# Optimization experiments

Measured on AMD Instinct MI355X. Metric: run time of the kernel, lower is better.

## Reference

```python
import jax, jax.numpy as jnp
import numpy as np

FG_THR = 0.7
BG_THR = 0.3
NUM_PER_IMAGE = 256
NUM_POS_MAX = int(NUM_PER_IMAGE * 0.5)  # positive_ratio = 0.5
BBOX_W = (1.0, 1.0, 1.0, 1.0)
BETA = 1.0 / 9.0


def _permute(t, C):
    # N x (A*C) x H x W -> N x (H*W*A) x C, matching RPNLoss.permute
    N, _, H, W = t.shape
    t = t.reshape(N, -1, C, H, W)
    t = jnp.transpose(t, (0, 3, 4, 1, 2))
    return t.reshape(N, -1, C)


def _iou(a, b):
    # a: [N,4], b: [M,4] -> [N,M] (with +1 box convention, as in source)
    x_tl = jnp.maximum(a[:, None, 0], b[None, :, 0])
    y_tl = jnp.maximum(a[:, None, 1], b[None, :, 1])
    x_rb = jnp.minimum(a[:, None, 2], b[None, :, 2])
    y_rb = jnp.minimum(a[:, None, 3], b[None, :, 3])
    inter = jnp.clip(x_rb - x_tl + 1.0, 0.0) * jnp.clip(y_rb - y_tl + 1.0, 0.0)
    area1 = (a[:, 2] - a[:, 0] + 1.0) * (a[:, 3] - a[:, 1] + 1.0)
    area2 = (b[:, 2] - b[:, 0] + 1.0) * (b[:, 3] - b[:, 1] + 1.0)
    return inter / (area1[:, None] + area2[None, :] - inter)


def _encode(anchors, targets):
    ws = anchors[:, 2] - anchors[:, 0] + 1.0
    hs = anchors[:, 3] - anchors[:, 1] + 1.0
    x_ctr = anchors[:, 0] + 0.5 * ws
    y_ctr = anchors[:, 1] + 0.5 * hs
    t_ws = targets[:, 2] - targets[:, 0] + 1.0
    t_hs = targets[:, 3] - targets[:, 1] + 1.0
    t_x = targets[:, 0] + 0.5 * t_ws
    t_y = targets[:, 1] + 0.5 * t_hs
    wx, wy, ww, wh = BBOX_W
    tx = wx * (t_x - x_ctr) / ws
    ty = wy * (t_y - y_ctr) / hs
    tw = ww * jnp.log(t_ws / ws)
    th = wh * jnp.log(t_hs / hs)
    return jnp.stack([tx, ty, tw, th], axis=1)


def _bce_logits(l, t):
    return jnp.maximum(l, 0.0) - l * t + jnp.log1p(jnp.exp(-jnp.abs(l)))


def _per_image(anchor, logit, breg, size, target, key):
    N = anchor.shape[0]
    ious = _iou(anchor, target)  # [N, M]
    vals = ious.max(axis=1)
    ori = jnp.argmax(ious, axis=1).astype(jnp.int32)
    inds = jnp.where(vals < BG_THR, -1, ori)
    inds = jnp.where((vals >= BG_THR) & (vals < FG_THR), -2, inds)
    # low-quality matches: anchors achieving the per-target max IoU keep their argmax
    col_max = ious.max(axis=0)
    restore = (ious == col_max[None, :]).any(axis=1)
    inds = jnp.where(restore, ori, inds)
    # filter_anchors: keep anchors fully inside the image (size = (h, w))
    inside = (anchor[:, 0] >= 0) & (anchor[:, 1] >= 0) & \
             (anchor[:, 2] <= size[1] - 1.0) & (anchor[:, 3] <= size[0] - 1.0)
    inds = jnp.where(inside, inds, -2)

    pos = inds >= 0
    neg = inds == -1
    # random sampling via random priorities + fixed-size top_k with validity masks
    r = jax.random.uniform(key, (N,))
    pos_vals, pos_idx = jax.lax.top_k(jnp.where(pos, r, -1.0), NUM_POS_MAX)
    valid_pos = pos_vals >= 0.0
    num_pos = valid_pos.sum()
    neg_vals, neg_idx = jax.lax.top_k(jnp.where(neg, r, -1.0), NUM_PER_IMAGE)
    valid_neg = (neg_vals >= 0.0) & (jnp.arange(NUM_PER_IMAGE) < (NUM_PER_IMAGE - num_pos))

    # classification loss terms (BCE with logits); pos target 1, neg target 0
    vp = valid_pos.astype(logit.dtype)
    vn = valid_neg.astype(logit.dtype)
    cls_sum = jnp.sum(_bce_logits(logit[pos_idx], 1.0) * vp) + \
              jnp.sum(_bce_logits(logit[neg_idx], 0.0) * vn)
    count = num_pos + valid_neg.sum()

    m = jnp.clip(inds[pos_idx], 0, None)
    offsets = _encode(anchor[pos_idx], target[m])
    diff = jnp.abs(breg[pos_idx] - offsets)
    sl1 = jnp.where(diff < BETA, 0.5 * diff * diff / BETA, diff - 0.5 * BETA)
    reg_sum = jnp.sum(sl1 * vp[:, None])
    return cls_sum, count, reg_sum


def reference(anchors, logits, bbox_regs, sizes, targets):
    B = anchors.shape[0]
    log = _permute(logits, 1)[..., 0]      # [B, H*W*A]
    breg = _permute(bbox_regs, 4)          # [B, H*W*A, 4]
    keys = jax.random.split(jax.random.key(42), B)
    cls_s, cnt, reg_s = jax.vmap(_per_image)(anchors, log, breg, sizes, targets, keys)
    total = jnp.sum(cnt).astype(anchors.dtype)
    cls_loss = jnp.sum(cls_s) / total
    reg_loss = jnp.sum(reg_s) / total
    return jnp.stack([cls_loss, reg_loss])


def setup_inputs() -> dict:
    key = jax.random.key(0)
    ks = jax.random.split(key, 10)
    B, A, H, W, M = 4, 3, 168, 256, 32
    N = H * W * A
    IMG_H, IMG_W = 800.0, 1333.0
    x1 = jax.random.uniform(ks[0], (B, N)) * 1200.0
    y1 = jax.random.uniform(ks[1], (B, N)) * 700.0
    aw = jax.random.uniform(ks[2], (B, N)) * 300.0 + 16.0
    ah = jax.random.uniform(ks[3], (B, N)) * 300.0 + 16.0
    anchors = jnp.stack([x1, y1, x1 + aw, y1 + ah], axis=-1)  # some out of image -> filtered
    tx1 = jax.random.uniform(ks[4], (B, M)) * 1000.0
    ty1 = jax.random.uniform(ks[5], (B, M)) * 500.0
    tw = jax.random.uniform(ks[6], (B, M)) * 250.0 + 30.0
    th = jax.random.uniform(ks[7], (B, M)) * 200.0 + 30.0
    targets = jnp.stack([tx1, ty1, jnp.minimum(tx1 + tw, IMG_W - 1.0),
                         jnp.minimum(ty1 + th, IMG_H - 1.0)], axis=-1)
    logits = jax.random.normal(ks[8], (B, A, H, W), dtype=jnp.float32)
    bbox_regs = jax.random.normal(ks[9], (B, 4 * A, H, W), dtype=jnp.float32) * 0.1
    sizes = jnp.tile(jnp.array([IMG_H, IMG_W], dtype=jnp.float32), (B, 1))
    return {"anchors": anchors, "logits": logits, "bbox_regs": bbox_regs,
            "sizes": sizes, "targets": targets}
```

## Files before the change

### kernel.cpp

```cpp
#include <hip/hip_runtime.h>
#include <stdint.h>

#define Bn 4
#define An 3
#define Hn 168
#define Wn 256
#define Mn 32
#define HWn (Hn*Wn)
#define Nn (HWn*An)
#define POS_CAP 8192
#define BND_CAP 2048
#define NPERIM 256
#define NPOSMAX 128
#define FG_THR 0.7f
#define BG_THR 0.3f
#define BETA (1.0f/9.0f)

#define NBLK 126
#define APT 4
#define STRIDE (NBLK * 256)
#define SEG 1024
#define WPI (NBLK * 4)
#define HB 256
#define HSH 15
#define BSEGCAP 64

#define OFF_POSCNT 0
#define OFF_BOUND  8
#define OFF_NEED   12
#define OFF_COUNT  16
#define OFF_CLS    17
#define OFF_REG    18
#define OFF_KEYS   24
#define OFF_WMAX   32
#define OFF_PACKED 64544
#define OFF_NSEGC  1096736
#define OFF_BSEGC  1097240
#define OFF_PHIST  1097744
#define OFF_PLIST  1226768
#define OFF_BSEG   1292304
#define OFF_NLIST  1356816

__device__ __forceinline__ uint32_t rotl32(uint32_t v, int n) { return (v << n) | (v >> (32 - n)); }

__device__ __forceinline__ void tf2x32(uint32_t k0, uint32_t k1, uint32_t x0, uint32_t x1,
                                       uint32_t& o0, uint32_t& o1) {
    uint32_t k2 = k0 ^ k1 ^ 0x1BD11BDAu;
    x0 += k0; x1 += k1;
    x0 += x1; x1 = rotl32(x1, 13); x1 ^= x0;
    x0 += x1; x1 = rotl32(x1, 15); x1 ^= x0;
    x0 += x1; x1 = rotl32(x1, 26); x1 ^= x0;
    x0 += x1; x1 = rotl32(x1, 6);  x1 ^= x0;
    x0 += k1; x1 += k2 + 1u;
    x0 += x1; x1 = rotl32(x1, 17); x1 ^= x0;
    x0 += x1; x1 = rotl32(x1, 29); x1 ^= x0;
    x0 += x1; x1 = rotl32(x1, 16); x1 ^= x0;
    x0 += x1; x1 = rotl32(x1, 24); x1 ^= x0;
    x0 += k2; x1 += k0 + 2u;
    x0 += x1; x1 = rotl32(x1, 13); x1 ^= x0;
    x0 += x1; x1 = rotl32(x1, 15); x1 ^= x0;
    x0 += x1; x1 = rotl32(x1, 26); x1 ^= x0;
    x0 += x1; x1 = rotl32(x1, 6);  x1 ^= x0;
    x0 += k0; x1 += k1 + 3u;
    x0 += x1; x1 = rotl32(x1, 17); x1 ^= x0;
    x0 += x1; x1 = rotl32(x1, 29); x1 ^= x0;
    x0 += x1; x1 = rotl32(x1, 16); x1 ^= x0;
    x0 += x1; x1 = rotl32(x1, 24); x1 ^= x0;
    x0 += k1; x1 += k2 + 4u;
    x0 += x1; x1 = rotl32(x1, 13); x1 ^= x0;
    x0 += x1; x1 = rotl32(x1, 15); x1 ^= x0;
    x0 += x1; x1 = rotl32(x1, 26); x1 ^= x0;
    x0 += x1; x1 = rotl32(x1, 6);  x1 ^= x0;
    x0 += k2; x1 += k0 + 5u;
    o0 = x0; o1 = x1;
}

__device__ __forceinline__ uint32_t rng_m23(uint32_t k0, uint32_t k1, uint32_t i) {
    uint32_t o0, o1;
    tf2x32(k0, k1, 0u, i, o0, o1);
    return (o0 ^ o1) >> 9;
}

__device__ __forceinline__ float iou_one(float a0, float a1, float a2, float a3,
                                         float t0, float t1, float t2, float t3) {
    float xtl = fmaxf(a0, t0), ytl = fmaxf(a1, t1);
    float xrb = fminf(a2, t2), yrb = fminf(a3, t3);
    float iw = fmaxf(xrb - xtl + 1.0f, 0.0f);
    float ih = fmaxf(yrb - ytl + 1.0f, 0.0f);
    float inter = iw * ih;
    float area1 = (a2 - a0 + 1.0f) * (a3 - a1 + 1.0f);
    float area2 = (t2 - t0 + 1.0f) * (t3 - t1 + 1.0f);
    return inter * __builtin_amdgcn_rcpf(area1 + area2 - inter);
}

__global__ void __launch_bounds__(256) k1_colmax(const float* __restrict__ anchors,
                                                 const float* __restrict__ targets,
                                                 const float* __restrict__ sizes,
                                                 uint32_t* __restrict__ ws) {
    int b = blockIdx.y, j = blockIdx.x, tid = threadIdx.x;
    if (b == 0 && j == 0) {
        if (tid < 24) ws[tid] = 0u;
        if (tid == 0) {
            for (int bb = 0; bb < Bn; ++bb) {
                uint32_t o0, o1;
                tf2x32(0u, 42u, 0u, (uint32_t)bb, o0, o1);
                ws[OFF_KEYS + 2*bb] = o0; ws[OFF_KEYS + 2*bb + 1] = o1;
            }
        }
    }
    int lane = tid & 63;
    int w = j * 4 + (tid >> 6);
    int base = j * 256 + tid;
    float4 a[APT];
    #pragma unroll
    for (int k = 0; k < APT; ++k)
        a[k] = ((const float4*)anchors)[b * Nn + base + k * STRIDE];
    float rowmax[APT]; int ori[APT]; uint32_t eqm[APT];
    #pragma unroll
    for (int k = 0; k < APT; ++k) { rowmax[k] = -1.0f; ori[k] = 0; eqm[k] = 0u; }
    float mywm = 0.0f;
    #pragma unroll 4
    for (int t = 0; t < Mn; ++t) {
        float4 tv = ((const float4*)targets)[b * Mn + t];
        float iou[APT];
        float m0 = 0.0f;
        #pragma unroll
        for (int k = 0; k < APT; ++k) {
            iou[k] = iou_one(a[k].x, a[k].y, a[k].z, a[k].w, tv.x, tv.y, tv.z, tv.w);
            if (iou[k] > rowmax[k]) { rowmax[k] = iou[k]; ori[k] = t; }
            m0 = fmaxf(m0, iou[k]);
        }
        #pragma unroll
        for (int o = 32; o > 0; o >>= 1) m0 = fmaxf(m0, __shfl_xor(m0, o, 64));
        #pragma unroll
        for (int k = 0; k < APT; ++k)
            eqm[k] |= (iou[k] == m0) ? (1u << t) : 0u;
        mywm = (lane == t) ? m0 : mywm;
    }
    if (lane < Mn)
        ws[OFF_WMAX + ((size_t)b * WPI + w) * Mn + lane] = __float_as_uint(mywm);
    float sh = sizes[b * 2 + 0], sw = sizes[b * 2 + 1];
    #pragma unroll
    for (int k = 0; k < APT; ++k) {
        int i = base + k * STRIDE;
        uint32_t inside = (a[k].x >= 0.0f) && (a[k].y >= 0.0f) &&
                          (a[k].z <= sw - 1.0f) && (a[k].w <= sh - 1.0f);
        uint32_t flags = (uint32_t)ori[k] | (inside << 5) |
                         ((rowmax[k] >= FG_THR ? 1u : 0u) << 6) |
                         ((rowmax[k] <  BG_THR ? 1u : 0u) << 7);
        ((uint2*)(ws + OFF_PACKED))[(size_t)b * Nn + i] = make_uint2(eqm[k], flags);
    }
}

__global__ void __launch_bounds__(256) k2_cat(uint32_t* __restrict__ ws) {
    int b = blockIdx.y, j = blockIdx.x, tid = threadIdx.x;
    int lane = tid & 63;
    int w = j * 4 + (tid >> 6);
    __shared__ float cmf[Mn];
    __shared__ float redf[256];
    __shared__ uint32_t lh[HB];
    __shared__ uint32_t segcnt;
    {
        int t = tid & 31, sub = tid >> 5;
        float acc = 0.0f;
        for (int ww = sub; ww < WPI; ww += 8)
            acc = fmaxf(acc, __uint_as_float(ws[OFF_WMAX + ((size_t)b * WPI + ww) * Mn + t]));
        redf[tid] = acc;
        __syncthreads();
        if (sub == 0) {
            #pragma unroll
            for (int q = 1; q < 8; ++q) acc = fmaxf(acc, redf[t + 32 * q]);
            cmf[t] = acc;
        }
    }
    lh[tid] = 0u;
    if (tid == 0) segcnt = 0u;
    __syncthreads();
    float wmv = (lane < Mn)
        ? __uint_as_float(ws[OFF_WMAX + ((size_t)b * WPI + w) * Mn + lane]) : -1.0f;
    float cmv = (lane < Mn) ? cmf[lane] : 0.0f;
    uint32_t gmask = (uint32_t)__ballot(lane < Mn && wmv == cmv);

    uint32_t key0 = ws[OFF_KEYS + 2 * b], key1 = ws[OFF_KEYS + 2 * b + 1];
    unsigned long long lt_mask = (lane == 63) ? 0x7FFFFFFFFFFFFFFFull : ((1ull << lane) - 1ull);
    uint2* nseg = (uint2*)(ws + OFF_NLIST) + (size_t)(b * NBLK + j) * SEG;
    int base = j * 256 + tid;
    #pragma unroll
    for (int k = 0; k < APT; ++k) {
        int i = base + k * STRIDE;
        uint2 pk = ((const uint2*)(ws + OFF_PACKED))[(size_t)b * Nn + i];
        uint32_t ori = pk.y & 31u;
        bool inside = (pk.y >> 5) & 1u;
        bool gefg   = (pk.y >> 6) & 1u;
        bool ltbg   = (pk.y >> 7) & 1u;
        bool restore = (pk.x & gmask) != 0u;
        uint32_t cat = 0;
        if (inside) {
            if (restore || gefg) cat = 2;
            else if (ltbg) cat = 1;
        }
        uint32_t m = rng_m23(key0, key1, (uint32_t)i);
        unsigned long long pmask = __ballot(cat == 2u);
        if (pmask) {
            int leader = __ffsll((long long)pmask) - 1;
            uint32_t bb = 0;
            if (lane == leader) bb = atomicAdd(&ws[OFF_POSCNT + b], (uint32_t)__popcll(pmask));
            bb = __shfl(bb, leader, 64);
            if (cat == 2u) {
                uint32_t p = bb + (uint32_t)__popcll(pmask & lt_mask);
                if (p < POS_CAP)
                    ((uint2*)(ws + OFF_PLIST))[(size_t)b * POS_CAP + p] =
                        make_uint2(m, (uint32_t)i | (ori << 17));
            }
        }
        unsigned long long nmask = __ballot(cat == 1u);
        if (nmask) {
            int leader = __ffsll((long long)nmask) - 1;
            uint32_t bb = 0;
            if (lane == leader) bb = atomicAdd(&segcnt, (uint32_t)__popcll(nmask));
            bb = __shfl(bb, leader, 64);
            if (cat == 1u) {
                uint32_t p = bb + (uint32_t)__popcll(nmask & lt_mask);
                nseg[p] = make_uint2(m, (uint32_t)i);
                atomicAdd(&lh[m >> HSH], 1u);
            }
        }
    }
    __syncthreads();
    ws[OFF_PHIST + ((size_t)b * NBLK + j) * HB + tid] = lh[tid];
    if (tid == 0) ws[OFF_NSEGC + b * NBLK + j] = segcnt;
}

__global__ void __launch_bounds__(256) k25_bound(uint32_t* __restrict__ ws) {
    int b = blockIdx.x, t = threadIdx.x;
    __shared__ uint32_t csum[256];
    const uint32_t* ph = ws + OFF_PHIST + (size_t)b * NBLK * HB;
    uint32_t h = 0;
    for (int s = 0; s < NBLK; ++s) h += ph[s * HB + t];
    csum[t] = h;
    __syncthreads();
    for (int off = 1; off < 256; off <<= 1) {
        uint32_t mine = csum[t];
        uint32_t add = (t + off < 256) ? csum[t + off] : 0u;
        __syncthreads();
        csum[t] = mine + add;
        __syncthreads();
    }
    uint32_t pc = ws[OFF_POSCNT + b];
    int num_pos = (pc < (uint32_t)NPOSMAX) ? (int)pc : NPOSMAX;
    int k_neg = NPERIM - num_pos;
    uint32_t total = csum[0];
    if ((int)total < k_neg) {
        if (t == 0) {
            ws[OFF_BOUND + b] = 0xFFFFFFFFu;
            ws[OFF_NEED + b] = 0u;
            atomicAdd(&ws[OFF_COUNT], (uint32_t)(num_pos + (int)total));
        }
        return;
    }
    uint32_t incl = csum[t];
    uint32_t next = (t < 255) ? csum[t + 1] : 0u;
    if ((int)incl >= k_neg && (int)next < k_neg) {
        ws[OFF_BOUND + b] = (uint32_t)t;
        ws[OFF_NEED + b] = (uint32_t)(k_neg - (int)next);
        atomicAdd(&ws[OFF_COUNT], (uint32_t)(num_pos + k_neg));
    }
}

__global__ void __launch_bounds__(256) k3_neg(const float* __restrict__ logits,
                                              uint32_t* __restrict__ ws) {
    int b = blockIdx.y, j = blockIdx.x;
    int tid = threadIdx.x;
    __shared__ uint32_t bcnt;
    __shared__ float red[256];
    if (tid == 0) bcnt = 0u;
    __syncthreads();
    int bd = (int)(int32_t)ws[OFF_BOUND + b];
    int cnt = (int)ws[OFF_NSEGC + b * NBLK + j];
    const uint2* nseg = (const uint2*)(ws + OFF_NLIST) + (size_t)(b * NBLK + j) * SEG;
    uint2* bseg = (uint2*)(ws + OFF_BSEG) + (size_t)(b * NBLK + j) * BSEGCAP;
    float local = 0.0f;
    for (int idx = tid; idx < cnt; idx += 256) {
        uint2 e = nseg[idx];
        int bk = (int)(e.x >> HSH);
        if (bk > bd) {
            int i = (int)e.y;
            int a = i % An, hw = i / An;
            float l = logits[(b * An + a) * HWn + hw];
            local += fmaxf(l, 0.0f) + log1pf(expf(-fabsf(l)));
        } else if (bk == bd) {
            uint32_t q = atomicAdd(&bcnt, 1u);
            if (q < BSEGCAP) bseg[q] = e;
        }
    }
    red[tid] = local;
    __syncthreads();
    for (int s = 128; s > 0; s >>= 1) {
        if (tid < s) red[tid] += red[tid + s];
        __syncthreads();
    }
    if (tid == 0) {
        if (red[0] != 0.0f) atomicAdd((float*)&ws[OFF_CLS], red[0]);
        ws[OFF_BSEGC + b * NBLK + j] = (bcnt < BSEGCAP) ? bcnt : BSEGCAP;
    }
}

__device__ __forceinline__ bool sel_less(uint2 a, uint2 b) {
    return (a.x > b.x) || (a.x == b.x && a.y < b.y);
}

__device__ void bitonic_sort_shared(uint2* buf, int n) {
    for (int k = 2; k <= n; k <<= 1) {
        for (int j = k >> 1; j > 0; j >>= 1) {
            for (int t = (int)threadIdx.x; t < n; t += 256) {
                int ixj = t ^ j;
                if (ixj > t) {
                    uint2 x = buf[t], y = buf[ixj];
                    bool up = ((t & k) == 0);
                    bool sw = up ? sel_less(y, x) : sel_less(x, y);
                    if (sw) { buf[t] = y; buf[ixj] = x; }
                }
            }
            __syncthreads();
        }
    }
}

__global__ void __launch_bounds__(256) k4_final(const float* __restrict__ anchors,
                                                const float* __restrict__ targets,
                                                const float* __restrict__ logits,
                                                const float* __restrict__ bregs,
                                                uint32_t* __restrict__ ws) {
    int b = blockIdx.x, tid = threadIdx.x;
    __shared__ uint2 buf[BND_CAP];
    __shared__ float red[256];
    __shared__ uint32_t pre[128];
    float cls = 0.0f, reg = 0.0f;

    uint32_t pcu = ws[OFF_POSCNT + b];
    int pc = (pcu < (uint32_t)POS_CAP) ? (int)pcu : POS_CAP;
    const uint2* plist = (const uint2*)(ws + OFF_PLIST) + (size_t)b * POS_CAP;
    int psel = (pc < NPOSMAX) ? pc : NPOSMAX;
    bool use_buf = false;
    if (pc > NPOSMAX) {
        int n = (pc < BND_CAP) ? pc : BND_CAP;
        for (int t = tid; t < n; t += 256) buf[t] = plist[t];
        int npad = 1; while (npad < n) npad <<= 1;
        for (int t = tid; t < npad; t += 256) if (t >= n) buf[t] = make_uint2(0u, 0xFFFFFFFFu);
        __syncthreads();
        bitonic_sort_shared(buf, npad);
        use_buf = true;
        psel = (NPOSMAX < n) ? NPOSMAX : n;
    }
    for (int t = tid; t < psel; t += 256) {
        uint32_t packed = use_buf ? buf[t].y : plist[t].y;
        int i = (int)(packed & 0x1FFFFu);
        int ori = (int)(packed >> 17);
        int a = i % An, hw = i / An;
        float l = logits[(b * An + a) * HWn + hw];
        cls += fmaxf(l, 0.0f) - l + log1pf(expf(-fabsf(l)));
        float4 av = ((const float4*)anchors)[b * Nn + i];
        float4 tv = ((const float4*)targets)[b * Mn + ori];
        float aws = av.z - av.x + 1.0f, ahs = av.w - av.y + 1.0f;
        float axc = av.x + 0.5f * aws, ayc = av.y + 0.5f * ahs;
        float tws = tv.z - tv.x + 1.0f, ths = tv.w - tv.y + 1.0f;
        float txc = tv.x + 0.5f * tws, tyc = tv.y + 0.5f * ths;
        float off0 = (txc - axc) / aws;
        float off1 = (tyc - ayc) / ahs;
        float off2 = logf(tws / aws);
        float off3 = logf(ths / ahs);
        float br0 = bregs[(b * 12 + a * 4 + 0) * HWn + hw];
        float br1 = bregs[(b * 12 + a * 4 + 1) * HWn + hw];
        float br2 = bregs[(b * 12 + a * 4 + 2) * HWn + hw];
        float br3 = bregs[(b * 12 + a * 4 + 3) * HWn + hw];
        float d;
        d = fabsf(br0 - off0); reg += (d < BETA) ? 0.5f * d * d / BETA : d - 0.5f * BETA;
        d = fabsf(br1 - off1); reg += (d < BETA) ? 0.5f * d * d / BETA : d - 0.5f * BETA;
        d = fabsf(br2 - off2); reg += (d < BETA) ? 0.5f * d * d / BETA : d - 0.5f * BETA;
        d = fabsf(br3 - off3); reg += (d < BETA) ? 0.5f * d * d / BETA : d - 0.5f * BETA;
    }
    __syncthreads();

    int need = (int)ws[OFF_NEED + b];
    if (need > 0) {
        uint32_t c = 0;
        if (tid < 128) {
            c = (tid < NBLK) ? ws[OFF_BSEGC + b * NBLK + tid] : 0u;
            pre[tid] = c;
        }
        __syncthreads();
        for (int off = 1; off < 128; off <<= 1) {
            uint32_t v = 0;
            if (tid < 128) { v = pre[tid]; if (tid >= off) v += pre[tid - off]; }
            __syncthreads();
            if (tid < 128) pre[tid] = v;
            __syncthreads();
        }
        int nb = (int)pre[127];
        if (nb > BND_CAP) nb = BND_CAP;
        if (tid < NBLK && c > 0) {
            uint32_t o0 = pre[tid] - c;
            const uint2* bs = (const uint2*)(ws + OFF_BSEG) + (size_t)(b * NBLK + tid) * BSEGCAP;
            for (uint32_t q = 0; q < c; ++q)
                if (o0 + q < (uint32_t)BND_CAP) buf[o0 + q] = bs[q];
        }
        int npad = 1; while (npad < nb) npad <<= 1;
        for (int t = tid; t < npad; t += 256) if (t >= nb) buf[t] = make_uint2(0u, 0xFFFFFFFFu);
        __syncthreads();
        bitonic_sort_shared(buf, npad);
        int sel = (need < nb) ? need : nb;
        for (int t = tid; t < sel; t += 256) {
            int i = (int)buf[t].y;
            int a = i % An, hw = i / An;
            float l = logits[(b * An + a) * HWn + hw];
            cls += fmaxf(l, 0.0f) + log1pf(expf(-fabsf(l)));
        }
    }

    red[tid] = cls;
    __syncthreads();
    for (int s = 128; s > 0; s >>= 1) {
        if (tid < s) red[tid] += red[tid + s];
        __syncthreads();
    }
    if (tid == 0 && red[0] != 0.0f) atomicAdd((float*)&ws[OFF_CLS], red[0]);
    __syncthreads();
    red[tid] = reg;
    __syncthreads();
    for (int s = 128; s > 0; s >>= 1) {
        if (tid < s) red[tid] += red[tid + s];
        __syncthreads();
    }
    if (tid == 0 && red[0] != 0.0f) atomicAdd((float*)&ws[OFF_REG], red[0]);
}

__global__ void k5_out(const uint32_t* __restrict__ ws, float* __restrict__ out) {
    if (blockIdx.x == 0 && threadIdx.x == 0) {
        float cnt = (float)ws[OFF_COUNT];
        out[0] = __uint_as_float(ws[OFF_CLS]) / cnt;
        out[1] = __uint_as_float(ws[OFF_REG]) / cnt;
    }
}

extern "C" void kernel_launch(void* const* d_in, const int* in_sizes, int n_in,
                              void* d_out, int out_size, void* d_ws, size_t ws_size,
                              hipStream_t stream) {
    const float* anchors = (const float*)d_in[0];
    const float* logits  = (const float*)d_in[1];
    const float* bregs   = (const float*)d_in[2];
    const float* sizes   = (const float*)d_in[3];
    const float* targets = (const float*)d_in[4];
    float* out = (float*)d_out;
    uint32_t* ws = (uint32_t*)d_ws;

    k1_colmax<<<dim3(NBLK, Bn), dim3(256), 0, stream>>>(anchors, targets, sizes, ws);
    k2_cat<<<dim3(NBLK, Bn), dim3(256), 0, stream>>>(ws);
    k25_bound<<<dim3(Bn), dim3(256), 0, stream>>>(ws);
    k3_neg<<<dim3(NBLK, Bn), dim3(256), 0, stream>>>(logits, ws);
    k4_final<<<dim3(Bn), dim3(256), 0, stream>>>(anchors, targets, logits, bregs, ws);
    k5_out<<<dim3(1), dim3(64), 0, stream>>>(ws, out);
}
```

Measured before the change: 163.5 us.

## Fuse boundary-bucket scan into negative kernel and replace bitonic sort with rank-select

Removes the separate k25_bound launch. Every k3_neg block now redundantly reduces the 126-segment histogram and scans it to find the boundary bucket itself. In k4_final, the shared-memory bitonic sorts for positives and boundary negatives are replaced by an O(n^2) rank count per element, keeping those with rank below the quota. This trades launch overhead and many barrier-separated sort passes for redundant histogram reads and quadratic comparisons, which could be costly when the candidate lists are large.

```diff
diff --git a/kernel.cpp b/kernel.cpp
--- a/kernel.cpp
+++ b/kernel.cpp
@@ -26,7 +26,6 @@
 #define BSEGCAP 64
 
 #define OFF_POSCNT 0
-#define OFF_BOUND  8
 #define OFF_NEED   12
 #define OFF_COUNT  16
 #define OFF_CLS    17
@@ -93,6 +92,10 @@
     return inter * __builtin_amdgcn_rcpf(area1 + area2 - inter);
 }
 
+__device__ __forceinline__ bool sel_less(uint2 a, uint2 b) {
+    return (a.x > b.x) || (a.x == b.x && a.y < b.y);
+}
+
 __global__ void __launch_bounds__(256) k1_colmax(const float* __restrict__ anchors,
                                                  const float* __restrict__ targets,
                                                  const float* __restrict__ sizes,
@@ -231,19 +234,24 @@
     if (tid == 0) ws[OFF_NSEGC + b * NBLK + j] = segcnt;
 }
 
-__global__ void __launch_bounds__(256) k25_bound(uint32_t* __restrict__ ws) {
-    int b = blockIdx.x, t = threadIdx.x;
+__global__ void __launch_bounds__(256) k3_neg(const float* __restrict__ logits,
+                                              uint32_t* __restrict__ ws) {
+    int b = blockIdx.y, j = blockIdx.x, tid = threadIdx.x;
     __shared__ uint32_t csum[256];
+    __shared__ float red[256];
+    __shared__ uint32_t bcnt;
+    __shared__ int s_bd, s_need;
+    if (tid == 0) { bcnt = 0u; s_bd = -1; s_need = 0; }
     const uint32_t* ph = ws + OFF_PHIST + (size_t)b * NBLK * HB;
     uint32_t h = 0;
-    for (int s = 0; s < NBLK; ++s) h += ph[s * HB + t];
-    csum[t] = h;
+    for (int s = 0; s < NBLK; ++s) h += ph[s * HB + tid];
+    csum[tid] = h;
     __syncthreads();
     for (int off = 1; off < 256; off <<= 1) {
-        uint32_t mine = csum[t];
-        uint32_t add = (t + off < 256) ? csum[t + off] : 0u;
-        __syncthreads();
-        csum[t] = mine + add;
+        uint32_t mine = csum[tid];
+        uint32_t add = (tid + off < 256) ? csum[tid + off] : 0u;
+        __syncthreads();
+        csum[tid] = mine + add;
         __syncthreads();
     }
     uint32_t pc = ws[OFF_POSCNT + b];
@@ -251,31 +259,25 @@
     int k_neg = NPERIM - num_pos;
     uint32_t total = csum[0];
     if ((int)total < k_neg) {
-        if (t == 0) {
-            ws[OFF_BOUND + b] = 0xFFFFFFFFu;
+        if (j == 0 && tid == 0) {
             ws[OFF_NEED + b] = 0u;
             atomicAdd(&ws[OFF_COUNT], (uint32_t)(num_pos + (int)total));
         }
-        return;
-    }
-    uint32_t incl = csum[t];
-    uint32_t next = (t < 255) ? csum[t + 1] : 0u;
-    if ((int)incl >= k_neg && (int)next < k_neg) {
-        ws[OFF_BOUND + b] = (uint32_t)t;
-        ws[OFF_NEED + b] = (uint32_t)(k_neg - (int)next);
-        atomicAdd(&ws[OFF_COUNT], (uint32_t)(num_pos + k_neg));
-    }
-}
-
-__global__ void __launch_bounds__(256) k3_neg(const float* __restrict__ logits,
-                                              uint32_t* __restrict__ ws) {
-    int b = blockIdx.y, j = blockIdx.x;
-    int tid = threadIdx.x;
-    __shared__ uint32_t bcnt;
-    __shared__ float red[256];
-    if (tid == 0) bcnt = 0u;
-    __syncthreads();
-    int bd = (int)(int32_t)ws[OFF_BOUND + b];
+    } else {
+        uint32_t incl = csum[tid];
+        uint32_t next = (tid < 255) ? csum[tid + 1] : 0u;
+        if ((int)incl >= k_neg && (int)next < k_neg) {
+            s_bd = tid;
+            s_need = k_neg - (int)next;
+            if (j == 0) {
+                ws[OFF_NEED + b] = (uint32_t)(k_neg - (int)next);
+                atomicAdd(&ws[OFF_COUNT], (uint32_t)(num_pos + k_neg));
+            }
+        }
+    }
+    __syncthreads();
+    int bd = s_bd;
+
     int cnt = (int)ws[OFF_NSEGC + b * NBLK + j];
     const uint2* nseg = (const uint2*)(ws + OFF_NLIST) + (size_t)(b * NBLK + j) * SEG;
     uint2* bseg = (uint2*)(ws + OFF_BSEG) + (size_t)(b * NBLK + j) * BSEGCAP;
@@ -305,27 +307,6 @@
     }
 }
 
-__device__ __forceinline__ bool sel_less(uint2 a, uint2 b) {
-    return (a.x > b.x) || (a.x == b.x && a.y < b.y);
-}
-
-__device__ void bitonic_sort_shared(uint2* buf, int n) {
-    for (int k = 2; k <= n; k <<= 1) {
-        for (int j = k >> 1; j > 0; j >>= 1) {
-            for (int t = (int)threadIdx.x; t < n; t += 256) {
-                int ixj = t ^ j;
-                if (ixj > t) {
-                    uint2 x = buf[t], y = buf[ixj];
-                    bool up = ((t & k) == 0);
-                    bool sw = up ? sel_less(y, x) : sel_less(x, y);
-                    if (sw) { buf[t] = y; buf[ixj] = x; }
-                }
-            }
-            __syncthreads();
-        }
-    }
-}
-
 __global__ void __launch_bounds__(256) k4_final(const float* __restrict__ anchors,
                                                 const float* __restrict__ targets,
                                                 const float* __restrict__ logits,
@@ -340,44 +321,47 @@
     uint32_t pcu = ws[OFF_POSCNT + b];
     int pc = (pcu < (uint32_t)POS_CAP) ? (int)pcu : POS_CAP;
     const uint2* plist = (const uint2*)(ws + OFF_PLIST) + (size_t)b * POS_CAP;
-    int psel = (pc < NPOSMAX) ? pc : NPOSMAX;
-    bool use_buf = false;
-    if (pc > NPOSMAX) {
-        int n = (pc < BND_CAP) ? pc : BND_CAP;
+    bool ranked = (pc > NPOSMAX);
+    int n = pc;
+    if (ranked) {
+        n = (pc < BND_CAP) ? pc : BND_CAP;
         for (int t = tid; t < n; t += 256) buf[t] = plist[t];
-        int npad = 1; while (npad < n) npad <<= 1;
-        for (int t = tid; t < npad; t += 256) if (t >= n) buf[t] = make_uint2(0u, 0xFFFFFFFFu);
-        __syncthreads();
-        bitonic_sort_shared(buf, npad);
-        use_buf = true;
-        psel = (NPOSMAX < n) ? NPOSMAX : n;
-    }
-    for (int t = tid; t < psel; t += 256) {
-        uint32_t packed = use_buf ? buf[t].y : plist[t].y;
-        int i = (int)(packed & 0x1FFFFu);
-        int ori = (int)(packed >> 17);
-        int a = i % An, hw = i / An;
-        float l = logits[(b * An + a) * HWn + hw];
-        cls += fmaxf(l, 0.0f) - l + log1pf(expf(-fabsf(l)));
-        float4 av = ((const float4*)anchors)[b * Nn + i];
-        float4 tv = ((const float4*)targets)[b * Mn + ori];
-        float aws = av.z - av.x + 1.0f, ahs = av.w - av.y + 1.0f;
-        float axc = av.x + 0.5f * aws, ayc = av.y + 0.5f * ahs;
-        float tws = tv.z - tv.x + 1.0f, ths = tv.w - tv.y + 1.0f;
-        float txc = tv.x + 0.5f * tws, tyc = tv.y + 0.5f * ths;
-        float off0 = (txc - axc) / aws;
-        float off1 = (tyc - ayc) / ahs;
-        float off2 = logf(tws / aws);
-        float off3 = logf(ths / ahs);
-        float br0 = bregs[(b * 12 + a * 4 + 0) * HWn + hw];
-        float br1 = bregs[(b * 12 + a * 4 + 1) * HWn + hw];
-        float br2 = bregs[(b * 12 + a * 4 + 2) * HWn + hw];
-        float br3 = bregs[(b * 12 + a * 4 + 3) * HWn + hw];
-        float d;
-        d = fabsf(br0 - off0); reg += (d < BETA) ? 0.5f * d * d / BETA : d - 0.5f * BETA;
-        d = fabsf(br1 - off1); reg += (d < BETA) ? 0.5f * d * d / BETA : d - 0.5f * BETA;
-        d = fabsf(br2 - off2); reg += (d < BETA) ? 0.5f * d * d / BETA : d - 0.5f * BETA;
-        d = fabsf(br3 - off3); reg += (d < BETA) ? 0.5f * d * d / BETA : d - 0.5f * BETA;
+        __syncthreads();
+    }
+    for (int t = tid; t < n; t += 256) {
+        uint2 e = ranked ? buf[t] : plist[t];
+        bool take = true;
+        if (ranked) {
+            int rank = 0;
+            for (int u = 0; u < n; ++u) rank += sel_less(buf[u], e) ? 1 : 0;
+            take = (rank < NPOSMAX);
+        }
+        if (take) {
+            int i = (int)(e.y & 0x1FFFFu);
+            int ori = (int)(e.y >> 17);
+            int a = i % An, hw = i / An;
+            float l = logits[(b * An + a) * HWn + hw];
+            cls += fmaxf(l, 0.0f) - l + log1pf(expf(-fabsf(l)));
+            float4 av = ((const float4*)anchors)[b * Nn + i];
+            float4 tv = ((const float4*)targets)[b * Mn + ori];
+            float aws = av.z - av.x + 1.0f, ahs = av.w - av.y + 1.0f;
+            float axc = av.x + 0.5f * aws, ayc = av.y + 0.5f * ahs;
+            float tws = tv.z - tv.x + 1.0f, ths = tv.w - tv.y + 1.0f;
+            float txc = tv.x + 0.5f * tws, tyc = tv.y + 0.5f * ths;
+            float off0 = (txc - axc) / aws;
+            float off1 = (tyc - ayc) / ahs;
+            float off2 = logf(tws / aws);
+            float off3 = logf(ths / ahs);
+            float br0 = bregs[(b * 12 + a * 4 + 0) * HWn + hw];
+            float br1 = bregs[(b * 12 + a * 4 + 1) * HWn + hw];
+            float br2 = bregs[(b * 12 + a * 4 + 2) * HWn + hw];
+            float br3 = bregs[(b * 12 + a * 4 + 3) * HWn + hw];
+            float d;
+            d = fabsf(br0 - off0); reg += (d < BETA) ? 0.5f * d * d / BETA : d - 0.5f * BETA;
+            d = fabsf(br1 - off1); reg += (d < BETA) ? 0.5f * d * d / BETA : d - 0.5f * BETA;
+            d = fabsf(br2 - off2); reg += (d < BETA) ? 0.5f * d * d / BETA : d - 0.5f * BETA;
+            d = fabsf(br3 - off3); reg += (d < BETA) ? 0.5f * d * d / BETA : d - 0.5f * BETA;
+        }
     }
     __syncthreads();
 
@@ -404,16 +388,17 @@
             for (uint32_t q = 0; q < c; ++q)
                 if (o0 + q < (uint32_t)BND_CAP) buf[o0 + q] = bs[q];
         }
-        int npad = 1; while (npad < nb) npad <<= 1;
-        for (int t = tid; t < npad; t += 256) if (t >= nb) buf[t] = make_uint2(0u, 0xFFFFFFFFu);
-        __syncthreads();
-        bitonic_sort_shared(buf, npad);
-        int sel = (need < nb) ? need : nb;
-        for (int t = tid; t < sel; t += 256) {
-            int i = (int)buf[t].y;
-            int a = i % An, hw = i / An;
-            float l = logits[(b * An + a) * HWn + hw];
-            cls += fmaxf(l, 0.0f) + log1pf(expf(-fabsf(l)));
+        __syncthreads();
+        for (int t = tid; t < nb; t += 256) {
+            uint2 e = buf[t];
+            int rank = 0;
+            for (int u = 0; u < nb; ++u) rank += sel_less(buf[u], e) ? 1 : 0;
+            if (rank < need) {
+                int i = (int)e.y;
+                int a = i % An, hw = i / An;
+                float l = logits[(b * An + a) * HWn + hw];
+                cls += fmaxf(l, 0.0f) + log1pf(expf(-fabsf(l)));
+            }
         }
     }
 
@@ -455,7 +440,6 @@
 
     k1_colmax<<<dim3(NBLK, Bn), dim3(256), 0, stream>>>(anchors, targets, sizes, ws);
     k2_cat<<<dim3(NBLK, Bn), dim3(256), 0, stream>>>(ws);
-    k25_bound<<<dim3(Bn), dim3(256), 0, stream>>>(ws);
     k3_neg<<<dim3(NBLK, Bn), dim3(256), 0, stream>>>(logits, ws);
     k4_final<<<dim3(Bn), dim3(256), 0, stream>>>(anchors, targets, logits, bregs, ws);
     k5_out<<<dim3(1), dim3(64), 0, stream>>>(ws, out);
```

Result: no change. 164.4 us (+0.5%).
